# Optimization experiments

Hardware: AMD Instinct MI355X
Metric: run time of the kernel (lower is better)

## Reference

```python
import jax, jax.numpy as jnp
import numpy as np

B, L, C, Q, H = 32, 2048, 512, 512, 1024

def setup_inputs() -> dict:
    key = jax.random.key(0)
    ks = jax.random.split(key, 8)
    query = jax.random.normal(ks[0], (B, Q), dtype=jnp.float32)
    context = jax.random.normal(ks[1], (B, L, C), dtype=jnp.float32)
    mapping_mask = jax.random.randint(ks[2], (B, L, 1), 0, 2).astype(jnp.float32)
    s = 0.02
    Wq = jax.random.normal(ks[3], (H, Q), dtype=jnp.float32) * s
    Wc = jax.random.normal(ks[4], (H, C), dtype=jnp.float32) * s
    bc = jnp.zeros((H,), dtype=jnp.float32)
    Wo = jax.random.normal(ks[5], (1, H), dtype=jnp.float32) * s
    bo = jnp.zeros((1,), dtype=jnp.float32)
    return {"query": query, "context": context, "mapping_mask": mapping_mask,
            "Wq": Wq, "Wc": Wc, "bc": bc, "Wo": Wo, "bo": bo}

def reference(query, context, mapping_mask, Wq, Wc, bc, Wo, bo):
    # res_q: [B,H], res_c: [B,L,H]
    res_q = query @ Wq.T
    res_c = jnp.einsum('blc,hc->blh', context, Wc) + bc
    tmp = jnp.tanh(res_q[:, None, :] + res_c)            # [B,L,H]
    weights_logit = jnp.einsum('blh,oh->blo', tmp, Wo) + bo  # [B,L,1]
    weights_exp = mapping_mask * jnp.exp(weights_logit)      # unnormalized, no max-subtract (faithful)
    weights = weights_exp / (weights_exp.sum(axis=1, keepdims=True) + 1e-5)
    output = jnp.einsum('blo,blc->boc', weights, context)[:, 0, :]  # bmm(w^T, ctx) -> squeeze
    return output, weights
```

## Files before the change

### kernel.cpp

```cpp
#include <hip/hip_runtime.h>

#define NB 32
#define LL 2048
#define CH 512
#define BQ 512
#define HH 1024
#define LDA 520

typedef __attribute__((ext_vector_type(8))) short bf16x8;
typedef __attribute__((ext_vector_type(16))) float f32x16;

__device__ __forceinline__ unsigned short f2bf(float x) {
  unsigned int u = __float_as_uint(x);
  u += 0x7FFFu + ((u >> 16) & 1u);
  return (unsigned short)(u >> 16);
}

__device__ __forceinline__ unsigned int cvt_pk_bf16(float a, float b) {
  unsigned int r;
  asm("v_cvt_pk_bf16_f32 %0, %1, %2" : "=v"(r) : "v"(a), "v"(b));
  return r;
}

__device__ __forceinline__ float fast_tanh(float x) {
  float e = __builtin_amdgcn_exp2f(x * 2.885390081777927f);
  return 1.0f - 2.0f * __builtin_amdgcn_rcpf(e + 1.0f);
}

__global__ __launch_bounds__(256) void k_resqc(const float* __restrict__ query,
                                               const float* __restrict__ Wq,
                                               const float* __restrict__ bc,
                                               float* __restrict__ resqc) {
  int gid = blockIdx.x * 256 + threadIdx.x;
  int b = gid >> 10, h = gid & 1023;
  const float4* q4 = (const float4*)(query + (size_t)b * BQ);
  const float4* w4 = (const float4*)(Wq + (size_t)h * BQ);
  float acc = 0.f;
#pragma unroll 4
  for (int i = 0; i < BQ / 4; ++i) {
    float4 a = q4[i], w = w4[i];
    acc += a.x * w.x + a.y * w.y + a.z * w.z + a.w * w.w;
  }
  resqc[gid] = acc + bc[h];
}

__global__ __launch_bounds__(256) void k_pack_wc(const float* __restrict__ Wc,
                                                 unsigned short* __restrict__ wcbp) {
  int gid = blockIdx.x * 256 + threadIdx.x;
  int lane = gid & 63, ks = (gid >> 6) & 31, cg = gid >> 11;
  int lo = lane & 31, hi = lane >> 5;
  const float4* s = (const float4*)(Wc + (size_t)(cg * 32 + lo) * CH + hi * 8 + ks * 16);
  float4 v0 = s[0], v1 = s[1];
  union { unsigned short s[8]; uint4 u; } p;
  p.s[0] = f2bf(v0.x); p.s[1] = f2bf(v0.y); p.s[2] = f2bf(v0.z); p.s[3] = f2bf(v0.w);
  p.s[4] = f2bf(v1.x); p.s[5] = f2bf(v1.y); p.s[6] = f2bf(v1.z); p.s[7] = f2bf(v1.w);
  ((uint4*)wcbp)[gid] = p.u;
}

__device__ __forceinline__ void stage_tile(const float* __restrict__ ctx,
                                           unsigned short* __restrict__ dst,
                                           int g, int t) {
  int b = g >> 5, row0 = (g & 31) << 6;
  const float4* src = (const float4*)(ctx + ((size_t)(b * LL + row0)) * CH);
#pragma unroll
  for (int i = 0; i < 16; ++i) {
    int f = i * 512 + t;
    int r = f >> 7, c4 = f & 127;
    float4 v = src[f];
    uint2 w;
    w.x = cvt_pk_bf16(v.x, v.y);
    w.y = cvt_pk_bf16(v.z, v.w);
    *(uint2*)(dst + r * LDA + c4 * 4) = w;
  }
}

__global__ __launch_bounds__(512, 2) void k_logits(const float* __restrict__ ctx,
                                                   const unsigned short* __restrict__ wcbp,
                                                   const float* __restrict__ resqc,
                                                   const float* __restrict__ Wo,
                                                   float* __restrict__ logits) {
  __shared__ unsigned short Alds[2][64 * LDA];
  __shared__ float lsum4[4][64];

  const int t = threadIdx.x;
  const int g0 = blockIdx.x * 4;

  if (t < 256) lsum4[t >> 6][t & 63] = 0.f;

  stage_tile(ctx, Alds[0], g0, t);
  __syncthreads();

  const int wave = t >> 6, lane = t & 63;
  const int lo = lane & 31, hi = lane >> 5;
  const int n0 = wave * 128;
  const uint4* bp = (const uint4*)wcbp + (size_t)(wave * 4) * 2048 + lane;
  float wo_[4];
#pragma unroll
  for (int n = 0; n < 4; ++n) wo_[n] = Wo[n0 + n * 32 + lo];

  for (int tt = 0; tt < 4; ++tt) {
    const int g = g0 + tt;
    const int b = g >> 5, row0 = (g & 31) << 6;
    const int cur = tt & 1;

    if (tt < 3) stage_tile(ctx, Alds[cur ^ 1], g + 1, t);

    const char* a0b = (const char*)(Alds[cur]) + lo * (LDA * 2) + hi * 16;

    f32x16 acc[2][4];
#pragma unroll
    for (int m = 0; m < 2; ++m)
#pragma unroll
      for (int n = 0; n < 4; ++n) acc[m][n] = (f32x16){0,0,0,0,0,0,0,0,0,0,0,0,0,0,0,0};

#pragma unroll 4
    for (int ks = 0; ks < 32; ++ks) {
      uint4 ub[4];
#pragma unroll
      for (int n = 0; n < 4; ++n) ub[n] = bp[(size_t)n * 2048 + ks * 64];
      bf16x8 fa[2];
#pragma unroll
      for (int m = 0; m < 2; ++m)
        fa[m] = *(const bf16x8*)(a0b + m * (32 * LDA * 2) + ks * 32);
#pragma unroll
      for (int m = 0; m < 2; ++m)
#pragma unroll
        for (int n = 0; n < 4; ++n) {
          bf16x8 fb;
          __builtin_memcpy(&fb, &ub[n], 16);
          acc[m][n] = __builtin_amdgcn_mfma_f32_32x32x16_bf16(fa[m], fb, acc[m][n], 0, 0, 0);
        }
    }

    float q_[4];
#pragma unroll
    for (int n = 0; n < 4; ++n) q_[n] = resqc[b * HH + n0 + n * 32 + lo];
    float v[32];
#pragma unroll
    for (int m = 0; m < 2; ++m)
#pragma unroll
      for (int r = 0; r < 16; ++r) {
        float s = 0.f;
#pragma unroll
        for (int n = 0; n < 4; ++n) s += wo_[n] * fast_tanh(acc[m][n][r] + q_[n]);
        v[m * 16 + r] = s;
      }
#pragma unroll
    for (int s = 16; s >= 1; s >>= 1) {
#pragma unroll
      for (int i = 0; i < s; ++i) {
        float a = v[i], c = v[i + s];
        float keep = (lo & s) ? c : a;
        float send = (lo & s) ? a : c;
        v[i] = keep + __shfl_xor(send, s, 64);
      }
    }
    int rr = lo & 15;
    int row = ((lo < 16) ? 0 : 32) + (rr & 3) + 8 * (rr >> 2) + 4 * hi;
    atomicAdd(&lsum4[tt][row], v[0]);

    __syncthreads();
    if (t < 64) logits[(size_t)b * LL + row0 + t] = lsum4[tt][t];
  }
}

__global__ __launch_bounds__(256) void k_weights(const float* __restrict__ mask,
                                                 const float* __restrict__ bo,
                                                 const float* __restrict__ logit,
                                                 float* __restrict__ wout) {
  __shared__ float red[4];
  int b = blockIdx.x, t = threadIdx.x;
  float bov = bo[0];
  float w[8];
  float s = 0.f;
#pragma unroll
  for (int i = 0; i < 8; ++i) {
    int l = t + 256 * i;
    float e = mask[b * LL + l] * __expf(logit[b * LL + l] + bov);
    w[i] = e; s += e;
  }
#pragma unroll
  for (int m = 32; m >= 1; m >>= 1) s += __shfl_xor(s, m, 64);
  int wave = t >> 6, lane = t & 63;
  if (lane == 0) red[wave] = s;
  __syncthreads();
  float inv = 1.0f / (red[0] + red[1] + red[2] + red[3] + 1e-5f);
#pragma unroll
  for (int i = 0; i < 8; ++i) wout[b * LL + t + 256 * i] = w[i] * inv;
}

__global__ __launch_bounds__(256) void k_output(const float* __restrict__ ctx,
                                                const float* __restrict__ weights,
                                                float* __restrict__ out) {
  __shared__ float wl[128];
  int bid = blockIdx.x;
  int b = bid >> 4, chunk = bid & 15;
  int t = threadIdx.x;
  int l0 = chunk * 128;
  if (t < 128) wl[t] = weights[b * LL + l0 + t];
  __syncthreads();
  const float2* c2 = (const float2*)(ctx + ((size_t)(b * LL + l0)) * CH) + t;
  float ax = 0.f, ay = 0.f;
#pragma unroll 4
  for (int l = 0; l < 128; ++l) {
    float wv = wl[l];
    float2 v = c2[(size_t)l * (CH / 2)];
    ax += wv * v.x; ay += wv * v.y;
  }
  atomicAdd(&out[b * CH + 2 * t], ax);
  atomicAdd(&out[b * CH + 2 * t + 1], ay);
}

extern "C" void kernel_launch(void* const* d_in, const int* in_sizes, int n_in,
                              void* d_out, int out_size, void* d_ws, size_t ws_size,
                              hipStream_t stream) {
  const float* query = (const float*)d_in[0];
  const float* ctx   = (const float*)d_in[1];
  const float* mask  = (const float*)d_in[2];
  const float* Wq    = (const float*)d_in[3];
  const float* Wc    = (const float*)d_in[4];
  const float* bc    = (const float*)d_in[5];
  const float* Wo    = (const float*)d_in[6];
  const float* bo    = (const float*)d_in[7];
  float* out = (float*)d_out;

  unsigned short* wcbp = (unsigned short*)d_ws;
  float* resqc = (float*)((char*)d_ws + (1 << 20));
  float* logit = (float*)((char*)d_ws + (1 << 20) + (1 << 17));
  float* wout = out + NB * CH;

  hipMemsetAsync(out, 0, NB * CH * sizeof(float), stream);
  k_resqc<<<128, 256, 0, stream>>>(query, Wq, bc, resqc);
  k_pack_wc<<<256, 256, 0, stream>>>(Wc, wcbp);
  k_logits<<<256, 512, 0, stream>>>(ctx, wcbp, resqc, Wo, logit);
  k_weights<<<32, 256, 0, stream>>>(mask, bo, logit, wout);
  k_output<<<512, 256, 0, stream>>>(ctx, wout, out);
}
```

Before: 140.1 us.

## Pre-pack context to bf16 MFMA layout and split logits GEMM across H tiles

Adds a kernel that converts the context tensor once to bf16 in the MFMA fragment layout in workspace. The logits GEMM now reads fragments straight from global memory with a 2D tile grid (128 rows by 128 H columns per block, XCD-aware block mapping) and accumulates partial logits via global atomics into a zeroed buffer. The output reduction also reads the packed bf16 context, which halves its read traffic. This adds a full extra pass writing 64MB of packed data, uses many more global atomics, and lowers output precision by reading context as bf16.

Result: slower. 157.5 us (+12.4%).

```diff
diff --git a/kernel.cpp b/kernel.cpp
--- a/kernel.cpp
+++ b/kernel.cpp
@@ -5,16 +5,9 @@
 #define CH 512
 #define BQ 512
 #define HH 1024
-#define LDA 520
 
 typedef __attribute__((ext_vector_type(8))) short bf16x8;
 typedef __attribute__((ext_vector_type(16))) float f32x16;
-
-__device__ __forceinline__ unsigned short f2bf(float x) {
-  unsigned int u = __float_as_uint(x);
-  u += 0x7FFFu + ((u >> 16) & 1u);
-  return (unsigned short)(u >> 16);
-}
 
 __device__ __forceinline__ unsigned int cvt_pk_bf16(float a, float b) {
   unsigned int r;
@@ -45,123 +38,114 @@
 }
 
 __global__ __launch_bounds__(256) void k_pack_wc(const float* __restrict__ Wc,
-                                                 unsigned short* __restrict__ wcbp) {
+                                                 uint4* __restrict__ wcbp) {
   int gid = blockIdx.x * 256 + threadIdx.x;
   int lane = gid & 63, ks = (gid >> 6) & 31, cg = gid >> 11;
   int lo = lane & 31, hi = lane >> 5;
   const float4* s = (const float4*)(Wc + (size_t)(cg * 32 + lo) * CH + hi * 8 + ks * 16);
   float4 v0 = s[0], v1 = s[1];
-  union { unsigned short s[8]; uint4 u; } p;
-  p.s[0] = f2bf(v0.x); p.s[1] = f2bf(v0.y); p.s[2] = f2bf(v0.z); p.s[3] = f2bf(v0.w);
-  p.s[4] = f2bf(v1.x); p.s[5] = f2bf(v1.y); p.s[6] = f2bf(v1.z); p.s[7] = f2bf(v1.w);
-  ((uint4*)wcbp)[gid] = p.u;
-}
-
-__device__ __forceinline__ void stage_tile(const float* __restrict__ ctx,
-                                           unsigned short* __restrict__ dst,
-                                           int g, int t) {
-  int b = g >> 5, row0 = (g & 31) << 6;
-  const float4* src = (const float4*)(ctx + ((size_t)(b * LL + row0)) * CH);
+  uint4 p;
+  p.x = cvt_pk_bf16(v0.x, v0.y);
+  p.y = cvt_pk_bf16(v0.z, v0.w);
+  p.z = cvt_pk_bf16(v1.x, v1.y);
+  p.w = cvt_pk_bf16(v1.z, v1.w);
+  wcbp[gid] = p;
+}
+
+__global__ __launch_bounds__(256) void k_pack_ctx_t(const float* __restrict__ ctx,
+                                                    uint4* __restrict__ apk) {
+  __shared__ unsigned short slds[32 * 520];
+  int g = blockIdx.x;
+  int t = threadIdx.x;
+  const float4* src = (const float4*)(ctx + (size_t)g * 32 * CH);
 #pragma unroll
   for (int i = 0; i < 16; ++i) {
-    int f = i * 512 + t;
-    int r = f >> 7, c4 = f & 127;
+    int f = i * 256 + t;
+    int row = f >> 7, c4 = f & 127;
     float4 v = src[f];
     uint2 w;
     w.x = cvt_pk_bf16(v.x, v.y);
     w.y = cvt_pk_bf16(v.z, v.w);
-    *(uint2*)(dst + r * LDA + c4 * 4) = w;
-  }
-}
-
-__global__ __launch_bounds__(512, 2) void k_logits(const float* __restrict__ ctx,
-                                                   const unsigned short* __restrict__ wcbp,
-                                                   const float* __restrict__ resqc,
-                                                   const float* __restrict__ Wo,
-                                                   float* __restrict__ logits) {
-  __shared__ unsigned short Alds[2][64 * LDA];
-  __shared__ float lsum4[4][64];
-
-  const int t = threadIdx.x;
-  const int g0 = blockIdx.x * 4;
-
-  if (t < 256) lsum4[t >> 6][t & 63] = 0.f;
-
-  stage_tile(ctx, Alds[0], g0, t);
+    *(uint2*)(slds + row * 520 + c4 * 4) = w;
+  }
   __syncthreads();
-
-  const int wave = t >> 6, lane = t & 63;
-  const int lo = lane & 31, hi = lane >> 5;
-  const int n0 = wave * 128;
-  const uint4* bp = (const uint4*)wcbp + (size_t)(wave * 4) * 2048 + lane;
-  float wo_[4];
-#pragma unroll
-  for (int n = 0; n < 4; ++n) wo_[n] = Wo[n0 + n * 32 + lo];
-
-  for (int tt = 0; tt < 4; ++tt) {
-    const int g = g0 + tt;
-    const int b = g >> 5, row0 = (g & 31) << 6;
-    const int cur = tt & 1;
-
-    if (tt < 3) stage_tile(ctx, Alds[cur ^ 1], g + 1, t);
-
-    const char* a0b = (const char*)(Alds[cur]) + lo * (LDA * 2) + hi * 16;
-
-    f32x16 acc[2][4];
-#pragma unroll
-    for (int m = 0; m < 2; ++m)
-#pragma unroll
-      for (int n = 0; n < 4; ++n) acc[m][n] = (f32x16){0,0,0,0,0,0,0,0,0,0,0,0,0,0,0,0};
+  uint4* dst = apk + (size_t)g * 2048;
+#pragma unroll
+  for (int i = 0; i < 8; ++i) {
+    int idx2 = i * 256 + t;
+    int ks = idx2 >> 6, lane2 = idx2 & 63;
+    int lo = lane2 & 31, hi = lane2 >> 5;
+    uint4 u = *(const uint4*)(slds + lo * 520 + ks * 16 + hi * 8);
+    dst[idx2] = u;
+  }
+}
+
+__global__ __launch_bounds__(256, 3) void k_logits_pk3(const uint4* __restrict__ apk,
+                                                       const uint4* __restrict__ bpk,
+                                                       const float* __restrict__ resqc,
+                                                       const float* __restrict__ Wo,
+                                                       float* __restrict__ logit) {
+  int bid = blockIdx.x;
+  int xcd = bid & 7, idx = bid >> 3;
+  int rb = xcd * 64 + (idx >> 3);
+  int cc = idx & 7;
+  int t = threadIdx.x;
+  int wv = t >> 6, lane = t & 63;
+  int wm = wv >> 1, wn = wv & 1;
+  int lo = lane & 31, hi = lane >> 5;
+  int b = rb >> 4;
+
+  const uint4* pa0 = apk + (size_t)(rb * 4 + wm * 2) * 2048 + lane;
+  const uint4* pa1 = pa0 + 2048;
+  const uint4* pb0 = bpk + (size_t)(cc * 4 + wn * 2) * 2048 + lane;
+  const uint4* pb1 = pb0 + 2048;
+
+  f32x16 acc[2][2];
+#pragma unroll
+  for (int m = 0; m < 2; ++m)
+#pragma unroll
+    for (int n = 0; n < 2; ++n) acc[m][n] = (f32x16){0,0,0,0,0,0,0,0,0,0,0,0,0,0,0,0};
 
 #pragma unroll 4
-    for (int ks = 0; ks < 32; ++ks) {
-      uint4 ub[4];
-#pragma unroll
-      for (int n = 0; n < 4; ++n) ub[n] = bp[(size_t)n * 2048 + ks * 64];
-      bf16x8 fa[2];
-#pragma unroll
-      for (int m = 0; m < 2; ++m)
-        fa[m] = *(const bf16x8*)(a0b + m * (32 * LDA * 2) + ks * 32);
-#pragma unroll
-      for (int m = 0; m < 2; ++m)
-#pragma unroll
-        for (int n = 0; n < 4; ++n) {
-          bf16x8 fb;
-          __builtin_memcpy(&fb, &ub[n], 16);
-          acc[m][n] = __builtin_amdgcn_mfma_f32_32x32x16_bf16(fa[m], fb, acc[m][n], 0, 0, 0);
-        }
+  for (int ks = 0; ks < 32; ++ks) {
+    uint4 ua0 = pa0[(size_t)ks * 64];
+    uint4 ua1 = pa1[(size_t)ks * 64];
+    uint4 ub0 = pb0[(size_t)ks * 64];
+    uint4 ub1 = pb1[(size_t)ks * 64];
+    bf16x8 fa0, fa1, fb0, fb1;
+    __builtin_memcpy(&fa0, &ua0, 16);
+    __builtin_memcpy(&fa1, &ua1, 16);
+    __builtin_memcpy(&fb0, &ub0, 16);
+    __builtin_memcpy(&fb1, &ub1, 16);
+    acc[0][0] = __builtin_amdgcn_mfma_f32_32x32x16_bf16(fa0, fb0, acc[0][0], 0, 0, 0);
+    acc[0][1] = __builtin_amdgcn_mfma_f32_32x32x16_bf16(fa0, fb1, acc[0][1], 0, 0, 0);
+    acc[1][0] = __builtin_amdgcn_mfma_f32_32x32x16_bf16(fa1, fb0, acc[1][0], 0, 0, 0);
+    acc[1][1] = __builtin_amdgcn_mfma_f32_32x32x16_bf16(fa1, fb1, acc[1][1], 0, 0, 0);
+  }
+
+  int c0 = cc * 128 + wn * 64;
+  float q0 = resqc[b * HH + c0 + lo], q1 = resqc[b * HH + c0 + 32 + lo];
+  float w0 = Wo[c0 + lo],             w1 = Wo[c0 + 32 + lo];
+  float v[32];
+#pragma unroll
+  for (int m = 0; m < 2; ++m)
+#pragma unroll
+    for (int r = 0; r < 16; ++r)
+      v[m * 16 + r] = w0 * fast_tanh(acc[m][0][r] + q0)
+                    + w1 * fast_tanh(acc[m][1][r] + q1);
+#pragma unroll
+  for (int sdist = 16; sdist >= 1; sdist >>= 1) {
+#pragma unroll
+    for (int i = 0; i < sdist; ++i) {
+      float a = v[i], c = v[i + sdist];
+      float keep = (lo & sdist) ? c : a;
+      float send = (lo & sdist) ? a : c;
+      v[i] = keep + __shfl_xor(send, sdist, 64);
     }
-
-    float q_[4];
-#pragma unroll
-    for (int n = 0; n < 4; ++n) q_[n] = resqc[b * HH + n0 + n * 32 + lo];
-    float v[32];
-#pragma unroll
-    for (int m = 0; m < 2; ++m)
-#pragma unroll
-      for (int r = 0; r < 16; ++r) {
-        float s = 0.f;
-#pragma unroll
-        for (int n = 0; n < 4; ++n) s += wo_[n] * fast_tanh(acc[m][n][r] + q_[n]);
-        v[m * 16 + r] = s;
-      }
-#pragma unroll
-    for (int s = 16; s >= 1; s >>= 1) {
-#pragma unroll
-      for (int i = 0; i < s; ++i) {
-        float a = v[i], c = v[i + s];
-        float keep = (lo & s) ? c : a;
-        float send = (lo & s) ? a : c;
-        v[i] = keep + __shfl_xor(send, s, 64);
-      }
-    }
-    int rr = lo & 15;
-    int row = ((lo < 16) ? 0 : 32) + (rr & 3) + 8 * (rr >> 2) + 4 * hi;
-    atomicAdd(&lsum4[tt][row], v[0]);
-
-    __syncthreads();
-    if (t < 64) logits[(size_t)b * LL + row0 + t] = lsum4[tt][t];
-  }
+  }
+  int rr = lo & 15;
+  int row_local = (lo >> 4) * 32 + (rr & 3) + 8 * (rr >> 2) + 4 * hi;
+  atomicAdd(&logit[rb * 128 + wm * 64 + row_local], v[0]);
 }
 
 __global__ __launch_bounds__(256) void k_weights(const float* __restrict__ mask,
@@ -189,26 +173,36 @@
   for (int i = 0; i < 8; ++i) wout[b * LL + t + 256 * i] = w[i] * inv;
 }
 
-__global__ __launch_bounds__(256) void k_output(const float* __restrict__ ctx,
-                                                const float* __restrict__ weights,
-                                                float* __restrict__ out) {
-  __shared__ float wl[128];
+__global__ __launch_bounds__(512) void k_output_pk(const uint4* __restrict__ apk,
+                                                   const float* __restrict__ wout,
+                                                   float* __restrict__ out) {
   int bid = blockIdx.x;
-  int b = bid >> 4, chunk = bid & 15;
+  int b = bid >> 4, q = (bid >> 2) & 3, lc = bid & 3;
   int t = threadIdx.x;
-  int l0 = chunk * 128;
-  if (t < 128) wl[t] = weights[b * LL + l0 + t];
-  __syncthreads();
-  const float2* c2 = (const float2*)(ctx + ((size_t)(b * LL + l0)) * CH) + t;
-  float ax = 0.f, ay = 0.f;
+  int lane = t & 63, ks = q * 8 + (t >> 6);
+  int lo = lane & 31, hi = lane >> 5;
+  const uint4* pa = apk + (size_t)(b * 64 + lc * 16) * 2048 + (size_t)ks * 64 + lane;
+  const float* wp = wout + b * LL + lc * 512 + lo;
+  float a8[8] = {0,0,0,0,0,0,0,0};
 #pragma unroll 4
-  for (int l = 0; l < 128; ++l) {
-    float wv = wl[l];
-    float2 v = c2[(size_t)l * (CH / 2)];
-    ax += wv * v.x; ay += wv * v.y;
-  }
-  atomicAdd(&out[b * CH + 2 * t], ax);
-  atomicAdd(&out[b * CH + 2 * t + 1], ay);
+  for (int gg = 0; gg < 16; ++gg) {
+    uint4 u = pa[(size_t)gg * 2048];
+    float w = wp[gg * 32];
+    unsigned int uu[4] = {u.x, u.y, u.z, u.w};
+#pragma unroll
+    for (int j = 0; j < 4; ++j) {
+      a8[2 * j]     += w * __uint_as_float(uu[j] << 16);
+      a8[2 * j + 1] += w * __uint_as_float(uu[j] & 0xffff0000u);
+    }
+  }
+#pragma unroll
+  for (int m = 1; m <= 16; m <<= 1)
+#pragma unroll
+    for (int j = 0; j < 8; ++j) a8[j] += __shfl_xor(a8[j], m, 64);
+  if (lo == 0) {
+#pragma unroll
+    for (int j = 0; j < 8; ++j) atomicAdd(&out[b * CH + ks * 16 + hi * 8 + j], a8[j]);
+  }
 }
 
 extern "C" void kernel_launch(void* const* d_in, const int* in_sizes, int n_in,
@@ -224,15 +218,18 @@
   const float* bo    = (const float*)d_in[7];
   float* out = (float*)d_out;
 
-  unsigned short* wcbp = (unsigned short*)d_ws;
+  uint4* wcbp  = (uint4*)d_ws;
   float* resqc = (float*)((char*)d_ws + (1 << 20));
   float* logit = (float*)((char*)d_ws + (1 << 20) + (1 << 17));
+  uint4* apk   = (uint4*)((char*)d_ws + (2 << 20));
   float* wout = out + NB * CH;
 
   hipMemsetAsync(out, 0, NB * CH * sizeof(float), stream);
+  hipMemsetAsync(logit, 0, NB * LL * sizeof(float), stream);
   k_resqc<<<128, 256, 0, stream>>>(query, Wq, bc, resqc);
   k_pack_wc<<<256, 256, 0, stream>>>(Wc, wcbp);
-  k_logits<<<256, 512, 0, stream>>>(ctx, wcbp, resqc, Wo, logit);
+  k_pack_ctx_t<<<2048, 256, 0, stream>>>(ctx, apk);
+  k_logits_pk3<<<4096, 256, 0, stream>>>(apk, wcbp, resqc, Wo, logit);
   k_weights<<<32, 256, 0, stream>>>(mask, bo, logit, wout);
-  k_output<<<512, 256, 0, stream>>>(ctx, wout, out);
-}
+  k_output_pk<<<512, 512, 0, stream>>>(apk, wout, out);
+}
```
